# Optimization experiments

Hardware: AMD Instinct MI355X
Metric: run time of the kernel (lower is better)

## Reference

```python
import jax, jax.numpy as jnp
import numpy as np

B, N, CIN, H, E = 1, 20000, 128, 128, 320000


def setup_inputs() -> dict:
    key = jax.random.key(0)
    ks = jax.random.split(key, 16)
    x = jax.random.normal(ks[0], (B, N, CIN), jnp.float32)
    edge_index = jax.random.randint(ks[1], (2, E), 0, N, dtype=jnp.int64)
    edge_weight = jax.random.uniform(ks[2], (E,), jnp.float32)
    h = jax.random.normal(ks[3], (B, N, H), jnp.float32)
    c = jax.random.normal(ks[4], (B, N, H), jnp.float32)
    # GCN stack params, gate order [i, f, c, o]; 2 layers each (K=2)
    Wx0 = jax.random.normal(ks[5], (4, CIN, H), jnp.float32) / np.float32(np.sqrt(CIN))
    bx0 = jnp.zeros((4, H), jnp.float32)
    Wx1 = jax.random.normal(ks[6], (4, H, H), jnp.float32) / np.float32(np.sqrt(H))
    bx1 = jnp.zeros((4, H), jnp.float32)
    Wh0 = jax.random.normal(ks[7], (4, H, H), jnp.float32) / np.float32(np.sqrt(H))
    bh0 = jnp.zeros((4, H), jnp.float32)
    Wh1 = jax.random.normal(ks[8], (4, H, H), jnp.float32) / np.float32(np.sqrt(H))
    bh1 = jnp.zeros((4, H), jnp.float32)
    wc = jax.random.normal(ks[9], (3, H), jnp.float32) * 0.1  # peephole [i, f, o]
    bg = jnp.zeros((4, H), jnp.float32)  # gate biases [i, f, c, o]
    return dict(x=x, edge_index=edge_index, edge_weight=edge_weight, h=h, c=c,
                Wx0=Wx0, bx0=bx0, Wx1=Wx1, bx1=bx1,
                Wh0=Wh0, bh0=bh0, Wh1=Wh1, bh1=bh1, wc=wc, bg=bg)


def reference(x, edge_index, edge_weight, h, c,
              Wx0, bx0, Wx1, bx1, Wh0, bh0, Wh1, bh1, wc, bg):
    n = x.shape[1]
    src, dst = edge_index[0], edge_index[1]
    loop = jnp.arange(n)
    src2 = jnp.concatenate([src, loop])
    dst2 = jnp.concatenate([dst, loop])
    w2 = jnp.concatenate([edge_weight, jnp.ones((n,), edge_weight.dtype)])
    deg = jax.ops.segment_sum(w2, dst2, num_segments=n)
    dis = jnp.where(deg > 0, jax.lax.rsqrt(jnp.maximum(deg, 1e-12)), 0.0)
    norm = dis[src2] * w2 * dis[dst2]  # sym GCN norm with self loops

    def prop(t):  # t: [..., N, F] -> D^-1/2 (A+I) D^-1/2 t
        lead = t.shape[:-2]
        tf = t.reshape((-1,) + t.shape[-2:])
        m = tf[:, src2, :] * norm[None, :, None]
        agg = jax.vmap(lambda mm: jax.ops.segment_sum(mm, dst2, num_segments=n))(m)
        return agg.reshape(lead + agg.shape[-2:])

    def gcn4(t, W0, b0, W1, b1):  # 2-layer GCN, 4 gates at once
        a = prop(t)  # shared first aggregation: [B,N,F]
        h0 = jax.nn.relu(jnp.einsum('bnc,gch->gbnh', a, W0) + b0[:, None, None, :])
        a1 = prop(h0)  # [4,B,N,H]
        return jnp.einsum('gbnh,ghk->gbnk', a1, W1) + b1[:, None, None, :]

    G = gcn4(x, Wx0, bx0, Wx1, bx1) + gcn4(h, Wh0, bh0, Wh1, bh1)  # [4,B,N,H]
    I = jax.nn.sigmoid(G[0] + wc[0] * c + bg[0])
    F = jax.nn.sigmoid(G[1] + wc[1] * c + bg[1])
    T = jnp.tanh(G[2] + bg[2])
    Cn = F * c + I * T
    O = jax.nn.sigmoid(G[3] + wc[2] * Cn + bg[3])
    Hn = O * jnp.tanh(Cn)
    return (Hn, Cn)
```

## Files before the change

### kernel.cpp

```cpp
#include <hip/hip_runtime.h>
#include <hip/hip_bf16.h>
#include <stdint.h>

#define NN    20000
#define NP    20096
#define EE    320000
#define CH    128
#define GC    512
#define NHtot 2560000

typedef short bf16x8 __attribute__((ext_vector_type(8)));
typedef float f32x4  __attribute__((ext_vector_type(4)));

__device__ __forceinline__ unsigned short f2bf(float f) {
    __hip_bfloat16 b = __float2bfloat16(f);
    union { __hip_bfloat16 b; unsigned short u; } c; c.b = b; return c.u;
}
__device__ __forceinline__ void fma4(uint2 u, float n, float* acc) {
    union { unsigned int i; float f; } t;
    t.i = u.x << 16;         acc[0] += n * t.f;
    t.i = u.x & 0xffff0000u; acc[1] += n * t.f;
    t.i = u.y << 16;         acc[2] += n * t.f;
    t.i = u.y & 0xffff0000u; acc[3] += n * t.f;
}
__device__ __forceinline__ void tof4(uint2 u, float* f) {
    union { unsigned int i; float f; } t;
    t.i = u.x << 16;         f[0] = t.f;
    t.i = u.x & 0xffff0000u; f[1] = t.f;
    t.i = u.y << 16;         f[2] = t.f;
    t.i = u.y & 0xffff0000u; f[3] = t.f;
}
__device__ __forceinline__ float bfu(unsigned short u) {
    union { unsigned int i; float f; } t;
    t.i = (unsigned int)u << 16; return t.f;
}
__device__ __forceinline__ uint2 pack4(const float* f) {
    uint2 v;
    v.x = (unsigned int)f2bf(f[0]) | ((unsigned int)f2bf(f[1]) << 16);
    v.y = (unsigned int)f2bf(f[2]) | ((unsigned int)f2bf(f[3]) << 16);
    return v;
}
__device__ __forceinline__ void gload_lds16(const void* g, void* l) {
    __builtin_amdgcn_global_load_lds(
        (const __attribute__((address_space(1))) void*)g,
        (__attribute__((address_space(3))) void*)l, 16, 0, 0);
}

__global__ void k_cntprep(const int* __restrict__ ei, int* __restrict__ cnt,
                          const float* __restrict__ W0, const float* __restrict__ W1,
                          const float* __restrict__ W2, const float* __restrict__ W3,
                          unsigned short* __restrict__ T0, unsigned short* __restrict__ T1,
                          unsigned short* __restrict__ T2, unsigned short* __restrict__ T3,
                          const float* __restrict__ bx1, const float* __restrict__ bh1,
                          const float* __restrict__ bg, float* __restrict__ btot) {
    int bid = blockIdx.x;
    if (bid < EE / 256) {
        int e = bid * 256 + threadIdx.x;
        atomicAdd(&cnt[ei[EE + e]], 1);
        return;
    }
    int pid = bid - EE / 256;
    int z = pid >> 8, y = (pid >> 6) & 3, xb = pid & 63;
    if (z == 0 && y == 0 && xb < 2) {
        int f = xb * 256 + threadIdx.x;
        int g = f >> 7, hh = f & 127;
        int pos = ((hh >> 4) << 6) | (g << 4) | (hh & 15);
        btot[pos] = bx1[f] + bh1[f] + bg[f];
    }
    const float* W; unsigned short* T;
    switch (z) {
        case 0:  W = W0; T = T0; break;
        case 1:  W = W1; T = T1; break;
        case 2:  W = W2; T = T2; break;
        default: W = W3; T = T3; break;
    }
    int n = xb * 2 + (threadIdx.x >> 7);
    int k = threadIdx.x & 127;
    T[((size_t)y * 128 + n) * 128 + k] = f2bf(W[((size_t)y * 128 + k) * 128 + n]);
}

__global__ void k_scan1(const int* __restrict__ cnt, int* __restrict__ rowoff,
                        int* __restrict__ bsum) {
    __shared__ int wsum[4];
    int i = blockIdx.x * 256 + threadIdx.x;
    int self = (i < NN) ? cnt[i] : 0;
    int lane = threadIdx.x & 63, wid = threadIdx.x >> 6;
    int v = self;
    #pragma unroll
    for (int off = 1; off < 64; off <<= 1) {
        int u = __shfl_up(v, off);
        if (lane >= off) v += u;
    }
    if (lane == 63) wsum[wid] = v;
    __syncthreads();
    int wof = 0;
    for (int k = 0; k < wid; ++k) wof += wsum[k];
    if (i < NN) rowoff[i] = wof + v - self;
    if (threadIdx.x == 255) bsum[blockIdx.x] = wof + v;
}

__global__ void k_scan2(int* __restrict__ bsum) {
    int lane = threadIdx.x;
    int base = 0;
    for (int start = 0; start < 80; start += 64) {
        int i = start + lane;
        int self = (i < 80) ? bsum[i] : 0;
        int v = self;
        #pragma unroll
        for (int off = 1; off < 64; off <<= 1) {
            int u = __shfl_up(v, off);
            if (lane >= off) v += u;
        }
        if (i < 80) bsum[i] = base + v - self;
        base += __shfl(v, 63);
    }
}

__global__ void k_scan3(int* __restrict__ rowoff, const int* __restrict__ bsum,
                        int* __restrict__ cur) {
    int i = blockIdx.x * 256 + threadIdx.x;
    if (i < NN) {
        int v = rowoff[i] + bsum[i >> 8];
        rowoff[i] = v; cur[i] = v;
    }
    if (i == NN) rowoff[NN] = EE;
}

__global__ void k_scatter(const int* __restrict__ ei, const float* __restrict__ ew,
                          int* __restrict__ cur,
                          int* __restrict__ csrs, float* __restrict__ csrw) {
    int e = blockIdx.x * 256 + threadIdx.x;
    if (e >= EE) return;
    int s = ei[e], d = ei[EE + e];
    int p = atomicAdd(&cur[d], 1);
    csrs[p] = s; csrw[p] = ew[e];
}

__global__ __launch_bounds__(256) void k_degcast(
        const float* __restrict__ x, const float* __restrict__ h,
        const int* __restrict__ rowoff, const float* __restrict__ csrw,
        float* __restrict__ dis, unsigned short* __restrict__ xhb) {
    int wid = threadIdx.x >> 6, lane = threadIdx.x & 63;
    int w = blockIdx.x * 4 + wid;
    int e0 = rowoff[w], e1 = rowoff[w + 1];
    float s = 0.f;
    for (int e = e0 + lane; e < e1; e += 64) s += csrw[e];
    #pragma unroll
    for (int off = 32; off; off >>= 1) s += __shfl_xor(s, off);
    float dn = rsqrtf(fmaxf(1.0f + s, 1e-12f));
    if (lane == 0) dis[w] = dn;
    const float* src = (lane < 32) ? x + (size_t)w * CH + lane * 4
                                   : h + (size_t)w * CH + (lane - 32) * 4;
    float4 v = *(const float4*)src;
    float f[4] = { dn * v.x, dn * v.y, dn * v.z, dn * v.w };
    *(uint2*)(xhb + (size_t)w * 256 + lane * 4) = pack4(f);
}

__global__ __launch_bounds__(128) void k_prop256(
        const unsigned short* __restrict__ tab, unsigned short* __restrict__ o,
        const int* __restrict__ rowoff, const int* __restrict__ csrs,
        const float* __restrict__ csrw, const float* __restrict__ dis) {
    int w = blockIdx.x * 2 + (threadIdx.x >> 6);
    int lane = threadIdx.x & 63;
    const uint2* T2 = (const uint2*)tab;
    float acc[4];
    tof4(T2[(size_t)w * 64 + lane], acc);
    int e = rowoff[w], e1 = rowoff[w + 1];
    for (; e + 8 <= e1; e += 8) {
        int   s0 = csrs[e],   s1 = csrs[e+1], s2 = csrs[e+2], s3 = csrs[e+3];
        int   s4 = csrs[e+4], s5 = csrs[e+5], s6 = csrs[e+6], s7 = csrs[e+7];
        uint2 u0 = T2[(size_t)s0 * 64 + lane];
        uint2 u1 = T2[(size_t)s1 * 64 + lane];
        uint2 u2 = T2[(size_t)s2 * 64 + lane];
        uint2 u3 = T2[(size_t)s3 * 64 + lane];
        uint2 u4 = T2[(size_t)s4 * 64 + lane];
        uint2 u5 = T2[(size_t)s5 * 64 + lane];
        uint2 u6 = T2[(size_t)s6 * 64 + lane];
        uint2 u7 = T2[(size_t)s7 * 64 + lane];
        float n0 = csrw[e],   n1 = csrw[e+1], n2 = csrw[e+2], n3 = csrw[e+3];
        float n4 = csrw[e+4], n5 = csrw[e+5], n6 = csrw[e+6], n7 = csrw[e+7];
        fma4(u0, n0, acc); fma4(u1, n1, acc); fma4(u2, n2, acc); fma4(u3, n3, acc);
        fma4(u4, n4, acc); fma4(u5, n5, acc); fma4(u6, n6, acc); fma4(u7, n7, acc);
    }
    for (; e + 4 <= e1; e += 4) {
        int   s0 = csrs[e],   s1 = csrs[e+1], s2 = csrs[e+2], s3 = csrs[e+3];
        float n0 = csrw[e],   n1 = csrw[e+1], n2 = csrw[e+2], n3 = csrw[e+3];
        uint2 u0 = T2[(size_t)s0 * 64 + lane];
        uint2 u1 = T2[(size_t)s1 * 64 + lane];
        uint2 u2 = T2[(size_t)s2 * 64 + lane];
        uint2 u3 = T2[(size_t)s3 * 64 + lane];
        fma4(u0, n0, acc); fma4(u1, n1, acc); fma4(u2, n2, acc); fma4(u3, n3, acc);
    }
    for (; e < e1; ++e) {
        fma4(T2[(size_t)csrs[e] * 64 + lane], csrw[e], acc);
    }
    float dw = dis[w];
    #pragma unroll
    for (int j = 0; j < 4; ++j) acc[j] *= dw;
    ((uint2*)o)[(size_t)w * 64 + lane] = pack4(acc);
}

#define SWZ(r, c8) (((r) << 4) + ((c8) ^ ((r) & 15)))

__global__ __launch_bounds__(256) void k_gemm1(
        const unsigned short* __restrict__ A,
        const unsigned short* __restrict__ Wtx, const unsigned short* __restrict__ Wth,
        const float* __restrict__ bx0, const float* __restrict__ bh0,
        unsigned short* __restrict__ outx, unsigned short* __restrict__ outh) {
    __shared__ uint4 As[2048];
    __shared__ uint4 Bs[2048];
    const int side = blockIdx.z;
    const int aoff = side * 128;
    const unsigned short* Wt = side ? Wth : Wtx;
    const float* bias        = side ? bh0 : bx0;
    unsigned short* out      = side ? outh : outx;

    const int    g    = blockIdx.y;
    const size_t row0 = (size_t)blockIdx.x * 128;
    const int    t    = threadIdx.x;
    const int    wv   = t >> 6;
    const unsigned short* Wg = Wt + (size_t)g * 16384;

    #pragma unroll
    for (int p = 0; p < 8; ++p) {
        int id = t + 256 * p, r = id >> 4, cc = id & 15;
        int c8 = cc ^ (r & 15);
        gload_lds16(A + (row0 + r) * 256 + aoff + c8 * 8, &As[p * 256 + wv * 64]);
        gload_lds16(Wg + r * CH + c8 * 8,                 &Bs[p * 256 + wv * 64]);
    }
    __syncthreads();

    const int l = t & 63;
    const int m0 = (wv >> 1) * 64, n0 = (wv & 1) * 64;
    const int lm = l & 15, q = l >> 4;
    f32x4 acc[4][4];
    #pragma unroll
    for (int i = 0; i < 4; ++i)
        #pragma unroll
        for (int j = 0; j < 4; ++j) { acc[i][j][0]=0.f; acc[i][j][1]=0.f; acc[i][j][2]=0.f; acc[i][j][3]=0.f; }

    #pragma unroll
    for (int kc = 0; kc < 4; ++kc) {
        int c8 = kc * 4 + q;
        bf16x8 a[4], b[4];
        #pragma unroll
        for (int i = 0; i < 4; ++i) { int r = m0 + i * 16 + lm; a[i] = *(const bf16x8*)&As[SWZ(r, c8)]; }
        #pragma unroll
        for (int j = 0; j < 4; ++j) { int r = n0 + j * 16 + lm; b[j] = *(const bf16x8*)&Bs[SWZ(r, c8)]; }
        #pragma unroll
        for (int i = 0; i < 4; ++i)
            #pragma unroll
            for (int j = 0; j < 4; ++j)
                acc[i][j] = __builtin_amdgcn_mfma_f32_16x16x32_bf16(a[i], b[j], acc[i][j], 0, 0, 0);
    }

    #pragma unroll
    for (int j = 0; j < 4; ++j) {
        float bb = bias[g * CH + n0 + j * 16 + lm];
        #pragma unroll
        for (int i = 0; i < 4; ++i)
            #pragma unroll
            for (int r = 0; r < 4; ++r) {
                int rowl = m0 + i * 16 + q * 4 + r;
                int col  = n0 + j * 16 + lm;
                out[(row0 + rowl) * GC + g * CH + col] = f2bf(fmaxf(acc[i][j][r] + bb, 0.f));
            }
    }
}

__global__ __launch_bounds__(256) void k_gemm2(
        const unsigned short* __restrict__ A1, const unsigned short* __restrict__ A2,
        const unsigned short* __restrict__ Wt1, const unsigned short* __restrict__ Wt2,
        const float* __restrict__ dis, unsigned short* __restrict__ outS) {
    __shared__ uint4 As[2048];
    __shared__ uint4 Bs[2048];
    const int    g    = blockIdx.y;
    const size_t row0 = (size_t)blockIdx.x * 128;
    const int    t    = threadIdx.x;
    const int    wv   = t >> 6;
    const int l = t & 63;
    const int m0 = (wv >> 1) * 64, n0 = (wv & 1) * 64;
    const int lm = l & 15, q = l >> 4;
    f32x4 acc[4][4];
    #pragma unroll
    for (int i = 0; i < 4; ++i)
        #pragma unroll
        for (int j = 0; j < 4; ++j) { acc[i][j][0]=0.f; acc[i][j][1]=0.f; acc[i][j][2]=0.f; acc[i][j][3]=0.f; }

    for (int side = 0; side < 2; ++side) {
        if (side) __syncthreads();
        const unsigned short* Ap = side ? A2 : A1;
        const unsigned short* Wg = (side ? Wt2 : Wt1) + (size_t)g * 16384;
        #pragma unroll
        for (int p = 0; p < 8; ++p) {
            int id = t + 256 * p, r = id >> 4, cc = id & 15;
            int c8 = cc ^ (r & 15);
            gload_lds16(Ap + (row0 + r) * GC + g * CH + c8 * 8, &As[p * 256 + wv * 64]);
            gload_lds16(Wg + r * CH + c8 * 8,                   &Bs[p * 256 + wv * 64]);
        }
        __syncthreads();
        #pragma unroll
        for (int kc = 0; kc < 4; ++kc) {
            int c8 = kc * 4 + q;
            bf16x8 a[4], b[4];
            #pragma unroll
            for (int i = 0; i < 4; ++i) { int r = m0 + i * 16 + lm; a[i] = *(const bf16x8*)&As[SWZ(r, c8)]; }
            #pragma unroll
            for (int j = 0; j < 4; ++j) { int r = n0 + j * 16 + lm; b[j] = *(const bf16x8*)&Bs[SWZ(r, c8)]; }
            #pragma unroll
            for (int i = 0; i < 4; ++i)
                #pragma unroll
                for (int j = 0; j < 4; ++j)
                    acc[i][j] = __builtin_amdgcn_mfma_f32_16x16x32_bf16(a[i], b[j], acc[i][j], 0, 0, 0);
        }
    }

    #pragma unroll
    for (int j = 0; j < 4; ++j) {
        int fh = (n0 + j * 16) >> 4;
        #pragma unroll
        for (int i = 0; i < 4; ++i)
            #pragma unroll
            for (int r = 0; r < 4; ++r) {
                int rowl = m0 + i * 16 + q * 4 + r;
                float dr = dis[row0 + rowl];
                outS[(row0 + rowl) * GC + fh * 64 + g * 16 + lm] = f2bf(dr * acc[i][j][r]);
            }
    }
}

__global__ __launch_bounds__(256) void k_prop512c(
        const unsigned short* __restrict__ Sb, float* __restrict__ out,
        const int* __restrict__ rowoff, const int* __restrict__ csrs,
        const float* __restrict__ csrw, const float* __restrict__ dis,
        const float* __restrict__ c, const float* __restrict__ btot,
        const float* __restrict__ wc) {
    int chunk = blockIdx.x & 7;
    int w = (blockIdx.x >> 3) * 4 + (threadIdx.x >> 6);
    int l = threadIdx.x & 63;
    const unsigned short* Sp = Sb + (size_t)chunk * 64 + l;
    float acc = bfu(Sp[(size_t)w * GC]);
    int e = rowoff[w], e1 = rowoff[w + 1];
    for (; e + 8 <= e1; e += 8) {
        int s0 = csrs[e],   s1 = csrs[e+1], s2 = csrs[e+2], s3 = csrs[e+3];
        int s4 = csrs[e+4], s5 = csrs[e+5], s6 = csrs[e+6], s7 = csrs[e+7];
        unsigned short u0 = Sp[(size_t)s0 * GC];
        unsigned short u1 = Sp[(size_t)s1 * GC];
        unsigned short u2 = Sp[(size_t)s2 * GC];
        unsigned short u3 = Sp[(size_t)s3 * GC];
        unsigned short u4 = Sp[(size_t)s4 * GC];
        unsigned short u5 = Sp[(size_t)s5 * GC];
        unsigned short u6 = Sp[(size_t)s6 * GC];
        unsigned short u7 = Sp[(size_t)s7 * GC];
        float n0 = csrw[e],   n1 = csrw[e+1], n2 = csrw[e+2], n3 = csrw[e+3];
        float n4 = csrw[e+4], n5 = csrw[e+5], n6 = csrw[e+6], n7 = csrw[e+7];
        acc += n0 * bfu(u0); acc += n1 * bfu(u1); acc += n2 * bfu(u2); acc += n3 * bfu(u3);
        acc += n4 * bfu(u4); acc += n5 * bfu(u5); acc += n6 * bfu(u6); acc += n7 * bfu(u7);
    }
    for (; e + 4 <= e1; e += 4) {
        int s0 = csrs[e],   s1 = csrs[e+1], s2 = csrs[e+2], s3 = csrs[e+3];
        unsigned short u0 = Sp[(size_t)s0 * GC];
        unsigned short u1 = Sp[(size_t)s1 * GC];
        unsigned short u2 = Sp[(size_t)s2 * GC];
        unsigned short u3 = Sp[(size_t)s3 * GC];
        float n0 = csrw[e],   n1 = csrw[e+1], n2 = csrw[e+2], n3 = csrw[e+3];
        acc += n0 * bfu(u0); acc += n1 * bfu(u1); acc += n2 * bfu(u2); acc += n3 * bfu(u3);
    }
    for (; e < e1; ++e) {
        acc += csrw[e] * bfu(Sp[(size_t)csrs[e] * GC]);
    }
    float dw = dis[w];
    float v  = dw * acc + btot[chunk * 64 + l];
    float x1 = __shfl_xor(v, 16);
    float x2 = __shfl_xor(v, 32);
    float x3 = __shfl_xor(v, 48);
    if ((l >> 4) == 0) {
        int hh = chunk * 16 + (l & 15);
        float cv = c[(size_t)w * CH + hh];
        float I  = 1.f / (1.f + expf(-(v  + wc[hh]       * cv)));
        float F  = 1.f / (1.f + expf(-(x1 + wc[128 + hh] * cv)));
        float T  = tanhf(x2);
        float Cn = F * cv + I * T;
        float O  = 1.f / (1.f + expf(-(x3 + wc[256 + hh] * Cn)));
        out[(size_t)w * CH + hh]         = O * tanhf(Cn);
        out[NHtot + (size_t)w * CH + hh] = Cn;
    }
}

extern "C" void kernel_launch(void* const* d_in, const int* in_sizes, int n_in,
                              void* d_out, int out_size, void* d_ws, size_t ws_size,
                              hipStream_t stream) {
    (void)in_sizes; (void)n_in; (void)out_size; (void)ws_size;
    const float* x   = (const float*)d_in[0];
    const int*   ei  = (const int*)d_in[1];
    const float* ew  = (const float*)d_in[2];
    const float* h   = (const float*)d_in[3];
    const float* c   = (const float*)d_in[4];
    const float* Wx0 = (const float*)d_in[5];
    const float* bx0 = (const float*)d_in[6];
    const float* Wx1 = (const float*)d_in[7];
    const float* bx1 = (const float*)d_in[8];
    const float* Wh0 = (const float*)d_in[9];
    const float* bh0 = (const float*)d_in[10];
    const float* Wh1 = (const float*)d_in[11];
    const float* bh1 = (const float*)d_in[12];
    const float* wc  = (const float*)d_in[13];
    const float* bg  = (const float*)d_in[14];
    float* out = (float*)d_out;

    float* wsf  = (float*)d_ws;
    float* dis  = wsf;
    int*   cnt  = (int*)(wsf + 20480);
    int*   row  = (int*)(wsf + 40960);
    int*   cur  = (int*)(wsf + 61696);
    int*   bsum = (int*)(wsf + 82176);
    float* btot = wsf + 82432;
    int*   csrs = (int*)(wsf + 82944);
    float* csrw = wsf + 402944;
    unsigned short* Wt0x = (unsigned short*)(wsf + 722944);
    unsigned short* Wt0h = (unsigned short*)(wsf + 755712);
    unsigned short* Wt1x = (unsigned short*)(wsf + 788480);
    unsigned short* Wt1h = (unsigned short*)(wsf + 821248);
    unsigned short* xhb  = (unsigned short*)(wsf + 854016);
    unsigned short* axh  = (unsigned short*)(wsf + 3426304);
    unsigned short* h0x  = (unsigned short*)(wsf + 5998592);
    unsigned short* h0h  = (unsigned short*)(wsf + 11143168);
    unsigned short* Sb   = (unsigned short*)(wsf + 16287744);

    hipMemsetAsync(cnt, 0, 20480 * sizeof(int), stream);

    k_cntprep<<<EE / 256 + 1024, 256, 0, stream>>>(ei, cnt,
                                                   Wx0, Wh0, Wx1, Wh1,
                                                   Wt0x, Wt0h, Wt1x, Wt1h,
                                                   bx1, bh1, bg, btot);
    k_scan1  <<<80, 256, 0, stream>>>(cnt, row, bsum);
    k_scan2  <<<1, 64, 0, stream>>>(bsum);
    k_scan3  <<<80, 256, 0, stream>>>(row, bsum, cur);
    k_scatter<<<EE / 256, 256, 0, stream>>>(ei, ew, cur, csrs, csrw);

    k_degcast<<<NN / 4, 256, 0, stream>>>(x, h, row, csrw, dis, xhb);

    k_prop256<<<NN / 2, 128, 0, stream>>>(xhb, axh, row, csrs, csrw, dis);

    dim3 g1(NP / 128, 4, 2);
    k_gemm1<<<g1, 256, 0, stream>>>(axh, Wt0x, Wt0h, bx0, bh0, h0x, h0h);
    dim3 g2(NP / 128, 4);
    k_gemm2<<<g2, 256, 0, stream>>>(h0x, h0h, Wt1x, Wt1h, dis, Sb);

    k_prop512c<<<(NN / 4) * 8, 256, 0, stream>>>(Sb, out, row, csrs, csrw, dis, c, btot, wc);
}
```

Measured before the change: 305.7 us.

## Split edge lists across lane groups with 16-byte gathers in both propagation kernels

Both sparse propagation kernels now assign 8 lanes per feature chunk and spread edges across 8 lane groups. Each lane gathers a 16-byte vector holding 8 bf16 values, where before it loaded 2-byte or 8-byte elements, and a shuffle reduction then sums the partial results. This is meant to raise memory-level parallelism and load width for the irregular gathers, especially in the final 512-wide kernel, which used scalar ushort loads. The cost is extra cross-lane reductions, idle lanes on rows with few edges, and a reworked gate epilogue in which only 2 lanes per wave compute outputs.

```diff
diff --git a/kernel.cpp b/kernel.cpp
--- a/kernel.cpp
+++ b/kernel.cpp
@@ -23,6 +23,17 @@
     t.i = u.y << 16;         acc[2] += n * t.f;
     t.i = u.y & 0xffff0000u; acc[3] += n * t.f;
 }
+__device__ __forceinline__ void fma8(uint4 u, float n, float* acc) {
+    union { unsigned int i; float f; } t;
+    t.i = u.x << 16;         acc[0] += n * t.f;
+    t.i = u.x & 0xffff0000u; acc[1] += n * t.f;
+    t.i = u.y << 16;         acc[2] += n * t.f;
+    t.i = u.y & 0xffff0000u; acc[3] += n * t.f;
+    t.i = u.z << 16;         acc[4] += n * t.f;
+    t.i = u.z & 0xffff0000u; acc[5] += n * t.f;
+    t.i = u.w << 16;         acc[6] += n * t.f;
+    t.i = u.w & 0xffff0000u; acc[7] += n * t.f;
+}
 __device__ __forceinline__ void tof4(uint2 u, float* f) {
     union { unsigned int i; float f; } t;
     t.i = u.x << 16;         f[0] = t.f;
@@ -30,9 +41,16 @@
     t.i = u.y << 16;         f[2] = t.f;
     t.i = u.y & 0xffff0000u; f[3] = t.f;
 }
-__device__ __forceinline__ float bfu(unsigned short u) {
+__device__ __forceinline__ void tof8(uint4 u, float* f) {
     union { unsigned int i; float f; } t;
-    t.i = (unsigned int)u << 16; return t.f;
+    t.i = u.x << 16;         f[0] = t.f;
+    t.i = u.x & 0xffff0000u; f[1] = t.f;
+    t.i = u.y << 16;         f[2] = t.f;
+    t.i = u.y & 0xffff0000u; f[3] = t.f;
+    t.i = u.z << 16;         f[4] = t.f;
+    t.i = u.z & 0xffff0000u; f[5] = t.f;
+    t.i = u.w << 16;         f[6] = t.f;
+    t.i = u.w & 0xffff0000u; f[7] = t.f;
 }
 __device__ __forceinline__ uint2 pack4(const float* f) {
     uint2 v;
@@ -156,48 +174,49 @@
     *(uint2*)(xhb + (size_t)w * 256 + lane * 4) = pack4(f);
 }
 
-__global__ __launch_bounds__(128) void k_prop256(
+__global__ __launch_bounds__(256) void k_prop256c(
         const unsigned short* __restrict__ tab, unsigned short* __restrict__ o,
         const int* __restrict__ rowoff, const int* __restrict__ csrs,
         const float* __restrict__ csrw, const float* __restrict__ dis) {
-    int w = blockIdx.x * 2 + (threadIdx.x >> 6);
-    int lane = threadIdx.x & 63;
-    const uint2* T2 = (const uint2*)tab;
-    float acc[4];
-    tof4(T2[(size_t)w * 64 + lane], acc);
+    int chunk = blockIdx.x & 3;
+    int w = (blockIdx.x >> 2) * 4 + (threadIdx.x >> 6);
+    int l = threadIdx.x & 63, grp = l >> 3, li = l & 7;
+    const uint4* T4 = (const uint4*)tab;
+    int coff = chunk * 8 + li;
+    float acc[8];
+    #pragma unroll
+    for (int j = 0; j < 8; ++j) acc[j] = 0.f;
+    if (grp == 0) tof8(T4[(size_t)w * 32 + coff], acc);
     int e = rowoff[w], e1 = rowoff[w + 1];
+    for (; e + 16 <= e1; e += 16) {
+        int   sA = csrs[e + grp],  sB = csrs[e + 8 + grp];
+        float nA = csrw[e + grp],  nB = csrw[e + 8 + grp];
+        uint4 uA = T4[(size_t)sA * 32 + coff];
+        uint4 uB = T4[(size_t)sB * 32 + coff];
+        fma8(uA, nA, acc); fma8(uB, nB, acc);
+    }
     for (; e + 8 <= e1; e += 8) {
-        int   s0 = csrs[e],   s1 = csrs[e+1], s2 = csrs[e+2], s3 = csrs[e+3];
-        int   s4 = csrs[e+4], s5 = csrs[e+5], s6 = csrs[e+6], s7 = csrs[e+7];
-        uint2 u0 = T2[(size_t)s0 * 64 + lane];
-        uint2 u1 = T2[(size_t)s1 * 64 + lane];
-        uint2 u2 = T2[(size_t)s2 * 64 + lane];
-        uint2 u3 = T2[(size_t)s3 * 64 + lane];
-        uint2 u4 = T2[(size_t)s4 * 64 + lane];
-        uint2 u5 = T2[(size_t)s5 * 64 + lane];
-        uint2 u6 = T2[(size_t)s6 * 64 + lane];
-        uint2 u7 = T2[(size_t)s7 * 64 + lane];
-        float n0 = csrw[e],   n1 = csrw[e+1], n2 = csrw[e+2], n3 = csrw[e+3];
-        float n4 = csrw[e+4], n5 = csrw[e+5], n6 = csrw[e+6], n7 = csrw[e+7];
-        fma4(u0, n0, acc); fma4(u1, n1, acc); fma4(u2, n2, acc); fma4(u3, n3, acc);
-        fma4(u4, n4, acc); fma4(u5, n5, acc); fma4(u6, n6, acc); fma4(u7, n7, acc);
-    }
-    for (; e + 4 <= e1; e += 4) {
-        int   s0 = csrs[e],   s1 = csrs[e+1], s2 = csrs[e+2], s3 = csrs[e+3];
-        float n0 = csrw[e],   n1 = csrw[e+1], n2 = csrw[e+2], n3 = csrw[e+3];
-        uint2 u0 = T2[(size_t)s0 * 64 + lane];
-        uint2 u1 = T2[(size_t)s1 * 64 + lane];
-        uint2 u2 = T2[(size_t)s2 * 64 + lane];
-        uint2 u3 = T2[(size_t)s3 * 64 + lane];
-        fma4(u0, n0, acc); fma4(u1, n1, acc); fma4(u2, n2, acc); fma4(u3, n3, acc);
-    }
-    for (; e < e1; ++e) {
-        fma4(T2[(size_t)csrs[e] * 64 + lane], csrw[e], acc);
-    }
-    float dw = dis[w];
-    #pragma unroll
-    for (int j = 0; j < 4; ++j) acc[j] *= dw;
-    ((uint2*)o)[(size_t)w * 64 + lane] = pack4(acc);
+        int s = csrs[e + grp]; float n = csrw[e + grp];
+        fma8(T4[(size_t)s * 32 + coff], n, acc);
+    }
+    if (grp < e1 - e) {
+        int s = csrs[e + grp]; float n = csrw[e + grp];
+        fma8(T4[(size_t)s * 32 + coff], n, acc);
+    }
+    #pragma unroll
+    for (int j = 0; j < 8; ++j) {
+        acc[j] += __shfl_xor(acc[j], 8);
+        acc[j] += __shfl_xor(acc[j], 16);
+        acc[j] += __shfl_xor(acc[j], 32);
+    }
+    if (grp == 0) {
+        float dw = dis[w];
+        #pragma unroll
+        for (int j = 0; j < 8; ++j) acc[j] *= dw;
+        uint2 p0 = pack4(acc), p1 = pack4(acc + 4);
+        uint4 ov; ov.x = p0.x; ov.y = p0.y; ov.z = p1.x; ov.w = p1.y;
+        ((uint4*)o)[(size_t)w * 32 + coff] = ov;
+    }
 }
 
 #define SWZ(r, c8) (((r) << 4) + ((c8) ^ ((r) & 15)))
@@ -329,7 +348,7 @@
     }
 }
 
-__global__ __launch_bounds__(256) void k_prop512c(
+__global__ __launch_bounds__(256) void k_prop512v(
         const unsigned short* __restrict__ Sb, float* __restrict__ out,
         const int* __restrict__ rowoff, const int* __restrict__ csrs,
         const float* __restrict__ csrw, const float* __restrict__ dis,
@@ -337,53 +356,69 @@
         const float* __restrict__ wc) {
     int chunk = blockIdx.x & 7;
     int w = (blockIdx.x >> 3) * 4 + (threadIdx.x >> 6);
-    int l = threadIdx.x & 63;
-    const unsigned short* Sp = Sb + (size_t)chunk * 64 + l;
-    float acc = bfu(Sp[(size_t)w * GC]);
+    int l = threadIdx.x & 63, grp = l >> 3, li = l & 7;
+    const uint4* S4 = (const uint4*)Sb;
+    int coff = chunk * 8 + li;
+    float acc[8];
+    #pragma unroll
+    for (int j = 0; j < 8; ++j) acc[j] = 0.f;
+    if (grp == 0) tof8(S4[(size_t)w * 64 + coff], acc);
     int e = rowoff[w], e1 = rowoff[w + 1];
+    for (; e + 16 <= e1; e += 16) {
+        int   sA = csrs[e + grp],  sB = csrs[e + 8 + grp];
+        float nA = csrw[e + grp],  nB = csrw[e + 8 + grp];
+        uint4 uA = S4[(size_t)sA * 64 + coff];
+        uint4 uB = S4[(size_t)sB * 64 + coff];
+        fma8(uA, nA, acc); fma8(uB, nB, acc);
+    }
     for (; e + 8 <= e1; e += 8) {
-        int s0 = csrs[e],   s1 = csrs[e+1], s2 = csrs[e+2], s3 = csrs[e+3];
-        int s4 = csrs[e+4], s5 = csrs[e+5], s6 = csrs[e+6], s7 = csrs[e+7];
-        unsigned short u0 = Sp[(size_t)s0 * GC];
-        unsigned short u1 = Sp[(size_t)s1 * GC];
-        unsigned short u2 = Sp[(size_t)s2 * GC];
-        unsigned short u3 = Sp[(size_t)s3 * GC];
-        unsigned short u4 = Sp[(size_t)s4 * GC];
-        unsigned short u5 = Sp[(size_t)s5 * GC];
-        unsigned short u6 = Sp[(size_t)s6 * GC];
-        unsigned short u7 = Sp[(size_t)s7 * GC];
-        float n0 = csrw[e],   n1 = csrw[e+1], n2 = csrw[e+2], n3 = csrw[e+3];
-        float n4 = csrw[e+4], n5 = csrw[e+5], n6 = csrw[e+6], n7 = csrw[e+7];
-        acc += n0 * bfu(u0); acc += n1 * bfu(u1); acc += n2 * bfu(u2); acc += n3 * bfu(u3);
-        acc += n4 * bfu(u4); acc += n5 * bfu(u5); acc += n6 * bfu(u6); acc += n7 * bfu(u7);
-    }
-    for (; e + 4 <= e1; e += 4) {
-        int s0 = csrs[e],   s1 = csrs[e+1], s2 = csrs[e+2], s3 = csrs[e+3];
-        unsigned short u0 = Sp[(size_t)s0 * GC];
-        unsigned short u1 = Sp[(size_t)s1 * GC];
-        unsigned short u2 = Sp[(size_t)s2 * GC];
-        unsigned short u3 = Sp[(size_t)s3 * GC];
-        float n0 = csrw[e],   n1 = csrw[e+1], n2 = csrw[e+2], n3 = csrw[e+3];
-        acc += n0 * bfu(u0); acc += n1 * bfu(u1); acc += n2 * bfu(u2); acc += n3 * bfu(u3);
-    }
-    for (; e < e1; ++e) {
-        acc += csrw[e] * bfu(Sp[(size_t)csrs[e] * GC]);
+        int s = csrs[e + grp]; float n = csrw[e + grp];
+        fma8(S4[(size_t)s * 64 + coff], n, acc);
+    }
+    if (grp < e1 - e) {
+        int s = csrs[e + grp]; float n = csrw[e + grp];
+        fma8(S4[(size_t)s * 64 + coff], n, acc);
+    }
+    #pragma unroll
+    for (int j = 0; j < 8; ++j) {
+        acc[j] += __shfl_xor(acc[j], 8);
+        acc[j] += __shfl_xor(acc[j], 16);
+        acc[j] += __shfl_xor(acc[j], 32);
     }
     float dw = dis[w];
-    float v  = dw * acc + btot[chunk * 64 + l];
-    float x1 = __shfl_xor(v, 16);
-    float x2 = __shfl_xor(v, 32);
-    float x3 = __shfl_xor(v, 48);
-    if ((l >> 4) == 0) {
-        int hh = chunk * 16 + (l & 15);
-        float cv = c[(size_t)w * CH + hh];
-        float I  = 1.f / (1.f + expf(-(v  + wc[hh]       * cv)));
-        float F  = 1.f / (1.f + expf(-(x1 + wc[128 + hh] * cv)));
-        float T  = tanhf(x2);
-        float Cn = F * cv + I * T;
-        float O  = 1.f / (1.f + expf(-(x3 + wc[256 + hh] * Cn)));
-        out[(size_t)w * CH + hh]         = O * tanhf(Cn);
-        out[NHtot + (size_t)w * CH + hh] = Cn;
+    float btv[8];
+    *(float4*)&btv[0] = *(const float4*)(btot + chunk * 64 + li * 8);
+    *(float4*)&btv[4] = *(const float4*)(btot + chunk * 64 + li * 8 + 4);
+    float v0[8], x1[8], x2[8], x3[8];
+    #pragma unroll
+    for (int j = 0; j < 8; ++j) v0[j] = dw * acc[j] + btv[j];
+    #pragma unroll
+    for (int j = 0; j < 8; ++j) {
+        x1[j] = __shfl_xor(v0[j], 2);
+        x2[j] = __shfl_xor(v0[j], 4);
+        x3[j] = __shfl_xor(v0[j], 6);
+    }
+    if (grp == 0 && li < 2) {
+        int hh0 = chunk * 16 + li * 8;
+        const float* cp = c + (size_t)w * CH + hh0;
+        float hn[8], cn[8];
+        #pragma unroll
+        for (int j = 0; j < 8; ++j) {
+            int hh = hh0 + j;
+            float cv = cp[j];
+            float I  = 1.f / (1.f + expf(-(v0[j] + wc[hh]       * cv)));
+            float F  = 1.f / (1.f + expf(-(x1[j] + wc[128 + hh] * cv)));
+            float T  = tanhf(x2[j]);
+            float Cn = F * cv + I * T;
+            float O  = 1.f / (1.f + expf(-(x3[j] + wc[256 + hh] * Cn)));
+            hn[j] = O * tanhf(Cn); cn[j] = Cn;
+        }
+        float* op  = out + (size_t)w * CH + hh0;
+        float* op2 = out + NHtot + (size_t)w * CH + hh0;
+        *(float4*)op        = *(float4*)&hn[0];
+        *(float4*)(op + 4)  = *(float4*)&hn[4];
+        *(float4*)op2       = *(float4*)&cn[0];
+        *(float4*)(op2 + 4) = *(float4*)&cn[4];
     }
 }
 
@@ -440,12 +475,12 @@
 
     k_degcast<<<NN / 4, 256, 0, stream>>>(x, h, row, csrw, dis, xhb);
 
-    k_prop256<<<NN / 2, 128, 0, stream>>>(xhb, axh, row, csrs, csrw, dis);
+    k_prop256c<<<(NN / 4) * 4, 256, 0, stream>>>(xhb, axh, row, csrs, csrw, dis);
 
     dim3 g1(NP / 128, 4, 2);
     k_gemm1<<<g1, 256, 0, stream>>>(axh, Wt0x, Wt0h, bx0, bh0, h0x, h0h);
     dim3 g2(NP / 128, 4);
     k_gemm2<<<g2, 256, 0, stream>>>(h0x, h0h, Wt1x, Wt1h, dis, Sb);
 
-    k_prop512c<<<(NN / 4) * 8, 256, 0, stream>>>(Sb, out, row, csrs, csrw, dis, c, btot, wc);
-}
+    k_prop512v<<<(NN / 4) * 8, 256, 0, stream>>>(Sb, out, row, csrs, csrw, dis, c, btot, wc);
+}
```

New measurement: 430.0 us. 40.7% more time.
